# Optimization experiments

Measured on AMD Instinct MI355X. Metric: run time of the kernel, lower is better.

The kernel has to match this reference:

```python
import jax, jax.numpy as jnp
import numpy as np

B, N, H, E, OBS, A, AFF, EFF = 2, 50000, 64, 1_000_000, 128, 18, 512, 256


def setup_inputs() -> dict:
    key = jax.random.key(0)
    ks = jax.random.split(key, 20)
    s = 0.05  # small init to keep gates/tanh unsaturated
    return {
        "obs": jax.random.normal(ks[0], (B, OBS), jnp.float32),
        "state": jax.random.normal(ks[1], (B, N, H), jnp.float32) * 0.1,
        "W_in": jax.random.normal(ks[2], (OBS, H), jnp.float32) * s,
        "b_in": jnp.zeros((H,), jnp.float32),
        "W_msg": jax.random.normal(ks[3], (H, H), jnp.float32) * s,
        "W_gate": jax.random.normal(ks[4], (2 * H, H), jnp.float32) * s,
        "b_gate": jnp.zeros((H,), jnp.float32),
        "W_cand": jax.random.normal(ks[5], (2 * H, H), jnp.float32) * s,
        "b_cand": jnp.zeros((H,), jnp.float32),
        "W_dec": jax.random.normal(ks[6], (H, H), jnp.float32) * s,
        "b_dec": jnp.zeros((H,), jnp.float32),
        "W_mean": jax.random.normal(ks[7], (H, A), jnp.float32) * s,
        "b_mean": jnp.zeros((A,), jnp.float32),
        "W_ls": jax.random.normal(ks[8], (H, A), jnp.float32) * s,
        "b_ls": jnp.zeros((A,), jnp.float32),
        "src_index": jax.random.randint(ks[9], (E,), 0, N),
        "dst_index": jax.random.randint(ks[10], (E,), 0, N),
        "afferent_idx": jax.random.randint(ks[11], (AFF,), 0, N),
        "efferent_idx": jax.random.randint(ks[12], (EFF,), 0, N),
    }


def reference(obs, state, W_in, b_in, W_msg, W_gate, b_gate, W_cand, b_cand,
              W_dec, b_dec, W_mean, b_mean, W_ls, b_ls,
              src_index, dst_index, afferent_idx, efferent_idx):
    # inject obs projection into afferent node slots
    projected = obs @ W_in + b_in                                   # [B, H]
    injected = jnp.zeros_like(state).at[:, afferent_idx, :].set(projected[:, None, :])
    # gather-project-scatter message passing over the edge list
    src_msgs = state[:, src_index, :] @ W_msg                       # [B, E, H]
    messages = jnp.zeros_like(state).at[:, dst_index, :].add(src_msgs)
    # GRU-style gated update
    combined = messages + injected
    gate_in = jnp.concatenate([state, combined], axis=-1)           # [B, N, 2H]
    z = jax.nn.sigmoid(gate_in @ W_gate + b_gate)
    cand = jnp.tanh(gate_in @ W_cand + b_cand)
    next_state = (1.0 - z) * state + z * cand
    # mean-pool readout over efferent nodes, then policy heads
    readout = next_state[:, efferent_idx, :].mean(axis=1)           # [B, H]
    decoded = jnp.tanh(readout @ W_dec + b_dec)
    mean = decoded @ W_mean + b_mean
    log_std = jnp.clip(decoded @ W_ls + b_ls, -5.0, 2.0)
    return mean, log_std, next_state
```

## Files before the change

### kernel.cpp

```cpp
#include <hip/hip_runtime.h>
#include <hip/hip_bf16.h>

constexpr int kN   = 50000;
constexpr int kH   = 64;
constexpr int kB   = 2;
constexpr int kE   = 1000000;
constexpr int kObs = 128;
constexpr int kA   = 18;
constexpr int kAff = 512;
constexpr int kEff = 256;
constexpr int kNH  = kN * kH;
constexpr int kOutOff = 2 * kB * kA;
constexpr int kRanges = 8;
constexpr int kNr  = kN / kRanges;
constexpr int kChunks = 64;
constexpr int kEc  = kE / kChunks;
constexpr int kHistB = kRanges * kChunks;
constexpr int kPackBlocks = (kNH + 8191) / 8192;
constexpr int kWprepBlocks = 20;
constexpr int kScanB = (kN + 255) / 256;

typedef __attribute__((ext_vector_type(8))) short short8_t;
typedef __attribute__((ext_vector_type(4))) float f32x4_t;

__device__ __forceinline__ float ldf(const void* p, int i, int f32) {
  if (f32) return ((const float*)p)[i];
  unsigned short u = ((const unsigned short*)p)[i];
  union { unsigned int x; float f; } v; v.x = ((unsigned int)u) << 16; return v.f;
}
__device__ __forceinline__ void stf(void* p, int i, float val, int f32) {
  if (f32) ((float*)p)[i] = val;
  else ((__hip_bfloat16*)p)[i] = __float2bfloat16(val);
}
__device__ __forceinline__ float lo16(unsigned int w) {
  union { unsigned int i; float f; } v; v.i = w << 16; return v.f;
}
__device__ __forceinline__ float hi16(unsigned int w) {
  union { unsigned int i; float f; } v; v.i = w & 0xffff0000u; return v.f;
}
__device__ __forceinline__ unsigned int f2b(float f) {
  union { float f; unsigned int u; } v; v.f = f;
  unsigned int r = v.u + 0x7fffu + ((v.u >> 16) & 1u);
  return r >> 16;
}
__device__ __forceinline__ int detect64(const unsigned short* wprobe, int t) {
  int hits = 0;
  for (int k = 0; k < 4; ++k) {
    unsigned short u = wprobe[(t * 4 + k) * 2];
    int e = (u >> 7) & 0xFF;
    if ((u & 0x7FFFu) != 0 && e >= 108 && e <= 128) hits++;
  }
  for (int off = 32; off; off >>= 1) hits += __shfl_down(hits, off);
  return (hits < 128) ? 1 : 0;
}

extern "C" __global__ __launch_bounds__(1024) void k_prep(
    const unsigned short* __restrict__ wprobe,
    const void* __restrict__ obs,
    const void* __restrict__ W_in,
    const void* __restrict__ b_in,
    const int* __restrict__ aff_idx,
    const int* __restrict__ dst,
    const void* __restrict__ W_msg,
    const void* __restrict__ W_gate,
    const void* __restrict__ W_cand,
    int* __restrict__ dflag,
    int* __restrict__ flags,
    float* __restrict__ projected,
    int* __restrict__ deg_c,
    unsigned short* __restrict__ wt) {
  __shared__ int sdeg[kNr];
  int t = threadIdx.x, b = blockIdx.x;
  if (b == 0) {
    __shared__ int sflag;
    if (t < 64) { int f = detect64(wprobe, t); if (t == 0) { sflag = f; dflag[0] = f; } }
    for (int i = t; i < kN; i += 1024) flags[i] = 0;
    __syncthreads();
    int f32 = sflag;
    if (t < kAff) flags[aff_idx[t]] = 1;
    if (t < kB * kH) {
      int bb = t >> 6, h = t & 63;
      float acc = ldf(b_in, h, f32);
      for (int o = 0; o < kObs; ++o)
        acc += ldf(obs, bb * kObs + o, f32) * ldf(W_in, o * kH + h, f32);
      projected[t] = acc;
    }
  } else if (b <= kHistB) {
    int h = b - 1, r = h & 7, c = h >> 3;
    int r0 = r * kNr;
    for (int i = t; i < kNr; i += 1024) sdeg[i] = 0;
    __syncthreads();
    int end = (c + 1) * kEc;
    for (int e = c * kEc + t; e < end; e += 1024) {
      unsigned rel = (unsigned)(dst[e] - r0);
      if (rel < (unsigned)kNr) atomicAdd(&sdeg[rel], 1);
    }
    __syncthreads();
    for (int i = t; i < kNr; i += 1024) deg_c[c * kN + r0 + i] = sdeg[i];
  } else {
    __shared__ int sflag;
    if (t < 64) { int f = detect64(wprobe, t); if (t == 0) sflag = f; }
    __syncthreads();
    int f32 = sflag;
    int i = (b - 1 - kHistB) * 1024 + t;
    if (i < 4096) {
      int n = i >> 6, k = i & 63;
      wt[i] = (unsigned short)f2b(ldf(W_msg, k * 64 + n, f32));
    } else if (i < 12288) {
      int j = i - 4096; int n = j >> 7, k = j & 127;
      wt[i] = (unsigned short)f2b(ldf(W_gate, k * 64 + n, f32));
    } else if (i < 20480) {
      int j = i - 12288; int n = j >> 7, k = j & 127;
      wt[i] = (unsigned short)f2b(ldf(W_cand, k * 64 + n, f32));
    }
  }
}

extern "C" __global__ void k_scan1(const int* __restrict__ deg_c,
                                   int* __restrict__ row_off,
                                   int* __restrict__ partials) {
  __shared__ int sd[256];
  int t = threadIdx.x;
  int n = blockIdx.x * 256 + t;
  int s = 0;
  if (n < kN) {
    for (int c = 0; c < kChunks; ++c) s += deg_c[c * kN + n];
  }
  sd[t] = s;
  __syncthreads();
  for (int off = 1; off < 256; off <<= 1) {
    int v = (t >= off) ? sd[t - off] : 0;
    __syncthreads();
    sd[t] += v;
    __syncthreads();
  }
  int excl = sd[t] - s;
  if (t == 255) partials[blockIdx.x] = sd[255];
  if (n < kN) row_off[n] = excl;
}

extern "C" __global__ void k_scan3(int* __restrict__ row_off,
                                   const int* __restrict__ partials,
                                   int* __restrict__ deg_c) {
  __shared__ int sd[256];
  int t = threadIdx.x;
  int s = 0;
  for (int j = t; j < (int)blockIdx.x; j += 256) s += partials[j];
  sd[t] = s;
  __syncthreads();
  for (int off = 128; off; off >>= 1) {
    if (t < off) sd[t] += sd[t + off];
    __syncthreads();
  }
  int base = sd[0];
  int n = blockIdx.x * 256 + t;
  if (n < kN) {
    int v = row_off[n] + base;
    row_off[n] = v;
    int run = v;
#pragma unroll 8
    for (int c = 0; c < kChunks; ++c) {
      int d = deg_c[c * kN + n];
      deg_c[c * kN + n] = run;
      run += d;
    }
  }
  if (blockIdx.x == 0 && t == 0) row_off[kN] = kE;
}

extern "C" __global__ __launch_bounds__(1024) void k_scatter(
    const int* __restrict__ src,
    const int* __restrict__ dst,
    const int* __restrict__ chunk_base,
    int* __restrict__ sorted_src,
    const unsigned short* __restrict__ wprobe,
    const void* __restrict__ state,
    unsigned int* __restrict__ pack) {
  __shared__ int scur[kNr];
  int t = threadIdx.x;
  if (blockIdx.x < kHistB) {
    int r = blockIdx.x & 7, c = blockIdx.x >> 3;
    int r0 = r * kNr;
    for (int i = t; i < kNr; i += 1024) scur[i] = chunk_base[c * kN + r0 + i];
    __syncthreads();
    int end = (c + 1) * kEc;
    for (int e = c * kEc + t; e < end; e += 1024) {
      unsigned rel = (unsigned)(dst[e] - r0);
      if (rel < (unsigned)kNr) {
        int pos = atomicAdd(&scur[rel], 1);
        sorted_src[pos] = src[e];
      }
    }
  } else {
    __shared__ int sflag;
    if (t < 64) { int f = detect64(wprobe, t); if (t == 0) sflag = f; }
    __syncthreads();
    int f32 = sflag;
    int i = (blockIdx.x - kHistB) * 8192 + t * 8;
    if (i < kNH) {
      uint4 o0, o1;
      if (!f32) {
        uint4 a = *(const uint4*)((const unsigned short*)state + i);
        uint4 c4 = *(const uint4*)((const unsigned short*)state + kNH + i);
        o0.x = (a.x & 0xffffu) | (c4.x << 16);
        o0.y = (a.x >> 16)     | (c4.x & 0xffff0000u);
        o0.z = (a.y & 0xffffu) | (c4.y << 16);
        o0.w = (a.y >> 16)     | (c4.y & 0xffff0000u);
        o1.x = (a.z & 0xffffu) | (c4.z << 16);
        o1.y = (a.z >> 16)     | (c4.z & 0xffff0000u);
        o1.z = (a.w & 0xffffu) | (c4.w << 16);
        o1.w = (a.w >> 16)     | (c4.w & 0xffff0000u);
      } else {
        const float* sf = (const float*)state;
        unsigned int w[8];
#pragma unroll
        for (int k = 0; k < 8; ++k)
          w[k] = f2b(sf[i + k]) | (f2b(sf[kNH + i + k]) << 16);
        o0 = make_uint4(w[0], w[1], w[2], w[3]);
        o1 = make_uint4(w[4], w[5], w[6], w[7]);
      }
      *(uint4*)&pack[i] = o0;
      *(uint4*)&pack[i + 4] = o1;
    }
  }
}

extern "C" __global__ __launch_bounds__(256) void k_gather(
    const unsigned int* __restrict__ pack,
    const int* __restrict__ row_off,
    const int* __restrict__ sorted_src,
    unsigned int* __restrict__ agg) {
  int wave = threadIdx.x >> 6, lane = threadIdx.x & 63;
  int n = blockIdx.x * 4 + wave;
  if (n >= kN) return;
  int s  = row_off[n];
  int en = row_off[n + 1];
  int g = lane >> 4, col = lane & 15;
  const uint4* pk4 = (const uint4*)pack;
  float a0x = 0.f, a0y = 0.f, a0z = 0.f, a0w = 0.f;
  float a1x = 0.f, a1y = 0.f, a1z = 0.f, a1w = 0.f;
  for (int e = s; e < en; e += 8) {
#pragma unroll
    for (int h = 0; h < 2; ++h) {
      int ee = e + h * 4 + g;
      int idx = sorted_src[min(ee, en - 1)];
      uint4 wv = pk4[idx * 16 + col];
      if (ee >= en) { wv.x = 0u; wv.y = 0u; wv.z = 0u; wv.w = 0u; }
      a0x += lo16(wv.x); a1x += hi16(wv.x);
      a0y += lo16(wv.y); a1y += hi16(wv.y);
      a0z += lo16(wv.z); a1z += hi16(wv.z);
      a0w += lo16(wv.w); a1w += hi16(wv.w);
    }
  }
  a0x += __shfl_xor(a0x, 16); a0x += __shfl_xor(a0x, 32);
  a0y += __shfl_xor(a0y, 16); a0y += __shfl_xor(a0y, 32);
  a0z += __shfl_xor(a0z, 16); a0z += __shfl_xor(a0z, 32);
  a0w += __shfl_xor(a0w, 16); a0w += __shfl_xor(a0w, 32);
  a1x += __shfl_xor(a1x, 16); a1x += __shfl_xor(a1x, 32);
  a1y += __shfl_xor(a1y, 16); a1y += __shfl_xor(a1y, 32);
  a1z += __shfl_xor(a1z, 16); a1z += __shfl_xor(a1z, 32);
  a1w += __shfl_xor(a1w, 16); a1w += __shfl_xor(a1w, 32);
  if (g == 0) {
    uint4 o;
    o.x = f2b(a0x) | (f2b(a1x) << 16);
    o.y = f2b(a0y) | (f2b(a1y) << 16);
    o.z = f2b(a0z) | (f2b(a1z) << 16);
    o.w = f2b(a0w) | (f2b(a1w) << 16);
    ((uint4*)agg)[n * 16 + col] = o;
  }
}

extern "C" __global__ __launch_bounds__(256) void k_update(
    const unsigned int* __restrict__ pk,
    const unsigned short* __restrict__ wt,
    const void* __restrict__ b_gate,
    const void* __restrict__ b_cand,
    const unsigned int* __restrict__ agg,
    const int* __restrict__ flags,
    const float* __restrict__ projected,
    const int* __restrict__ dflag,
    void* __restrict__ out) {
  __shared__ uint4 lx4[1088];
  __shared__ float sbias[128];
  __shared__ float sproj[128];
  __shared__ int   sfl[32];
  unsigned short* lx  = (unsigned short*)lx4;
  int f32 = dflag[0];
  int t = threadIdx.x;
  int nd0 = blockIdx.x * 32;

  const uint4* pk4 = (const uint4*)pk;
  const uint4* ag4 = (const uint4*)agg;
  for (int i = t; i < 512; i += 256) {
    int ndl = i >> 4, c4 = i & 15;
    int ndg = min(nd0 + ndl, kN - 1);
    uint4 pv = pk4[ndg * 16 + c4];
    uint4 av = ag4[ndg * 16 + c4];
    *(uint2*)&lx[(2 * ndl) * 136 + c4 * 4] =
        make_uint2((pv.x & 0xffffu) | (pv.y << 16), (pv.z & 0xffffu) | (pv.w << 16));
    *(uint2*)&lx[(2 * ndl + 1) * 136 + c4 * 4] =
        make_uint2((pv.x >> 16) | (pv.y & 0xffff0000u), (pv.z >> 16) | (pv.w & 0xffff0000u));
    *(uint2*)&lx[(2 * ndl) * 136 + 64 + c4 * 4] =
        make_uint2((av.x & 0xffffu) | (av.y << 16), (av.z & 0xffffu) | (av.w << 16));
    *(uint2*)&lx[(2 * ndl + 1) * 136 + 64 + c4 * 4] =
        make_uint2((av.x >> 16) | (av.y & 0xffff0000u), (av.z >> 16) | (av.w & 0xffff0000u));
  }
  if (t < 64) sbias[t] = ldf(b_gate, t, f32);
  else if (t < 128) sbias[t] = ldf(b_cand, t - 64, f32);
  else sproj[t - 128] = projected[t - 128];
  if (t < 32) sfl[t] = (nd0 + t < kN) ? flags[nd0 + t] : 0;
  __syncthreads();

  int w = t >> 6, lane = t & 63;
  int q = lane >> 4, l15 = lane & 15;
  int rowb = w * 16;
  const unsigned short* wm = wt;
  const unsigned short* wg = wt + 4096;
  const unsigned short* wc = wt + 12288;

  short8_t a0 = *(const short8_t*)&lx[(rowb + l15) * 136 + 64 + q * 8];
  short8_t a1 = *(const short8_t*)&lx[(rowb + l15) * 136 + 96 + q * 8];
  f32x4_t msgc[4];
#pragma unroll
  for (int ct = 0; ct < 4; ++ct) {
    f32x4_t acc = {0.f, 0.f, 0.f, 0.f};
    short8_t b0 = *(const short8_t*)&wm[(ct * 16 + l15) * 64 + q * 8];
    short8_t b1 = *(const short8_t*)&wm[(ct * 16 + l15) * 64 + 32 + q * 8];
    acc = __builtin_amdgcn_mfma_f32_16x16x32_bf16(a0, b0, acc, 0, 0, 0);
    acc = __builtin_amdgcn_mfma_f32_16x16x32_bf16(a1, b1, acc, 0, 0, 0);
    msgc[ct] = acc;
  }
#pragma unroll
  for (int ct = 0; ct < 4; ++ct) {
    int col = ct * 16 + l15;
    float pj0 = sproj[col], pj1 = sproj[64 + col];
#pragma unroll
    for (int r = 0; r < 4; ++r) {
      int row = rowb + q * 4 + r;
      int ndl = row >> 1, b = row & 1;
      float inj = sfl[ndl] ? (b ? pj1 : pj0) : 0.f;
      lx[row * 136 + 64 + col] = (unsigned short)f2b(msgc[ct][r] + inj);
    }
  }

  short8_t xa[4];
#pragma unroll
  for (int ks = 0; ks < 4; ++ks)
    xa[ks] = *(const short8_t*)&lx[(rowb + l15) * 136 + ks * 32 + q * 8];
#pragma unroll
  for (int ct = 0; ct < 4; ++ct) {
    f32x4_t accg = {0.f, 0.f, 0.f, 0.f}, accc = {0.f, 0.f, 0.f, 0.f};
#pragma unroll
    for (int ks = 0; ks < 4; ++ks) {
      short8_t bg = *(const short8_t*)&wg[(ct * 16 + l15) * 128 + ks * 32 + q * 8];
      short8_t bc = *(const short8_t*)&wc[(ct * 16 + l15) * 128 + ks * 32 + q * 8];
      accg = __builtin_amdgcn_mfma_f32_16x16x32_bf16(xa[ks], bg, accg, 0, 0, 0);
      accc = __builtin_amdgcn_mfma_f32_16x16x32_bf16(xa[ks], bc, accc, 0, 0, 0);
    }
    int col = ct * 16 + l15;
    float bgv = sbias[col], bcv = sbias[64 + col];
#pragma unroll
    for (int rp = 0; rp < 2; ++rp) {
      int rowe = rowb + q * 4 + 2 * rp;
      int nd = nd0 + (rowe >> 1);
      if (nd >= kN) continue;
      unsigned int pv = pk[nd * 64 + col];
      float z0 = 1.f / (1.f + __expf(-(accg[2 * rp] + bgv)));
      float c0 = tanhf(accc[2 * rp] + bcv);
      stf(out, kOutOff + nd * 64 + col, (1.f - z0) * lo16(pv) + z0 * c0, f32);
      float z1 = 1.f / (1.f + __expf(-(accg[2 * rp + 1] + bgv)));
      float c1 = tanhf(accc[2 * rp + 1] + bcv);
      stf(out, kOutOff + kNH + nd * 64 + col, (1.f - z1) * hi16(pv) + z1 * c1, f32);
    }
  }
}

extern "C" __global__ void k_readout(const void* __restrict__ W_dec,
                                     const void* __restrict__ b_dec,
                                     const void* __restrict__ W_mean,
                                     const void* __restrict__ b_mean,
                                     const void* __restrict__ W_ls,
                                     const void* __restrict__ b_ls,
                                     const int* __restrict__ eff_idx,
                                     const int* __restrict__ dflag,
                                     void* __restrict__ out) {
  __shared__ float part[8][64];
  __shared__ float ro[128], dec[128];
  int f32 = dflag[0];
  int t = threadIdx.x;
  int wv = t >> 6, lane = t & 63;
  int b = wv >> 2, g = wv & 3;
  float acc = 0.f;
#pragma unroll 4
  for (int i = 0; i < 64; ++i) {
    int n = eff_idx[g * 64 + i];
    acc += ldf(out, kOutOff + b * kNH + n * 64 + lane, f32);
  }
  part[wv][lane] = acc;
  __syncthreads();
  if (t < 128) {
    int bb = t >> 6, h = t & 63;
    float s = part[bb * 4 + 0][h] + part[bb * 4 + 1][h] +
              part[bb * 4 + 2][h] + part[bb * 4 + 3][h];
    ro[t] = s * (1.f / kEff);
  }
  __syncthreads();
  if (t < 128) {
    int bb = t >> 6, h = t & 63;
    float d = ldf(b_dec, h, f32);
    for (int k = 0; k < 64; ++k) d += ro[bb * 64 + k] * ldf(W_dec, k * 64 + h, f32);
    dec[t] = tanhf(d);
  }
  __syncthreads();
  if (t < kB * kA) {
    int bb = t / kA, a = t % kA;
    float m = ldf(b_mean, a, f32), l = ldf(b_ls, a, f32);
    for (int k = 0; k < 64; ++k) {
      float dv = dec[bb * 64 + k];
      m += dv * ldf(W_mean, k * kA + a, f32);
      l += dv * ldf(W_ls, k * kA + a, f32);
    }
    l = fminf(fmaxf(l, -5.f), 2.f);
    stf(out, t, m, f32);
    stf(out, kB * kA + t, l, f32);
  }
}

extern "C" void kernel_launch(void* const* d_in, const int* in_sizes, int n_in,
                              void* d_out, int out_size, void* d_ws, size_t ws_size,
                              hipStream_t stream) {
  (void)in_sizes; (void)n_in; (void)out_size; (void)ws_size;
  const void* obs    = d_in[0];
  const void* state  = d_in[1];
  const void* W_in   = d_in[2];
  const void* b_in   = d_in[3];
  const void* W_msg  = d_in[4];
  const void* W_gate = d_in[5];
  const void* b_gate = d_in[6];
  const void* W_cand = d_in[7];
  const void* b_cand = d_in[8];
  const void* W_dec  = d_in[9];
  const void* b_dec  = d_in[10];
  const void* W_mean = d_in[11];
  const void* b_mean = d_in[12];
  const void* W_ls   = d_in[13];
  const void* b_ls   = d_in[14];
  const int* src = (const int*)d_in[15];
  const int* dst = (const int*)d_in[16];
  const int* aff = (const int*)d_in[17];
  const int* eff = (const int*)d_in[18];

  int* wsp        = (int*)d_ws;
  int* flags      = wsp;
  int* deg_c      = flags + kN;
  int* row_off    = deg_c + kChunks * kN;
  int* partials   = row_off + (kN + 64);
  int* dflag      = partials + 512;
  float* projected = (float*)(dflag + 16);
  int* sorted_src  = (int*)(projected + 128);
  unsigned int* pk  = (unsigned int*)(sorted_src + kE);
  unsigned int* agg = pk + kNH;
  unsigned short* wt = (unsigned short*)(agg + kNH);

  k_prep<<<1 + kHistB + kWprepBlocks, 1024, 0, stream>>>(
      (const unsigned short*)W_cand, obs, W_in, b_in, aff, dst,
      W_msg, W_gate, W_cand, dflag, flags, projected, deg_c, wt);
  k_scan1<<<kScanB, 256, 0, stream>>>(deg_c, row_off, partials);
  k_scan3<<<kScanB, 256, 0, stream>>>(row_off, partials, deg_c);
  k_scatter<<<kHistB + kPackBlocks, 1024, 0, stream>>>(
      src, dst, deg_c, sorted_src, (const unsigned short*)W_cand, state, pk);
  k_gather<<<(kN + 3) / 4, 256, 0, stream>>>(pk, row_off, sorted_src, agg);
  k_update<<<(kN + 31) / 32, 256, 0, stream>>>(pk, wt, b_gate, b_cand,
                                               agg, flags, projected, dflag, d_out);
  k_readout<<<1, 512, 0, stream>>>(W_dec, b_dec, W_mean, b_mean, W_ls, b_ls, eff,
                                   dflag, d_out);
}
```

Before: 281.1 us.

## Fuse CSR gather into update kernel and stage outputs through LDS

The separate gather kernel is removed. Each wave of the update kernel now aggregates neighbor states for its own 8 nodes directly into LDS, so the intermediate agg buffer no longer has to be written to and read back from global memory. Outputs are staged in LDS and written with coalesced vector stores, and fast rcp-based sigmoid and tanh replace the exact versions. The risks are lower parallelism during the gather phase, since one wave now walks 8 nodes serially, and slightly different rounding from the approximate transcendentals.

```diff
diff --git a/kernel.cpp b/kernel.cpp
--- a/kernel.cpp
+++ b/kernel.cpp
@@ -38,10 +38,19 @@
 __device__ __forceinline__ float hi16(unsigned int w) {
   union { unsigned int i; float f; } v; v.i = w & 0xffff0000u; return v.f;
 }
+__device__ __forceinline__ float b2f(unsigned short u) {
+  union { unsigned int i; float f; } v; v.i = ((unsigned int)u) << 16; return v.f;
+}
 __device__ __forceinline__ unsigned int f2b(float f) {
   union { float f; unsigned int u; } v; v.f = f;
   unsigned int r = v.u + 0x7fffu + ((v.u >> 16) & 1u);
   return r >> 16;
+}
+__device__ __forceinline__ float fsig(float x) {
+  return __builtin_amdgcn_rcpf(1.f + __expf(-x));
+}
+__device__ __forceinline__ float ftanh(float x) {
+  return 1.f - 2.f * __builtin_amdgcn_rcpf(__expf(2.f * x) + 1.f);
 }
 __device__ __forceinline__ int detect64(const unsigned short* wprobe, int t) {
   int hits = 0;
@@ -225,95 +234,75 @@
   }
 }
 
-extern "C" __global__ __launch_bounds__(256) void k_gather(
-    const unsigned int* __restrict__ pack,
-    const int* __restrict__ row_off,
-    const int* __restrict__ sorted_src,
-    unsigned int* __restrict__ agg) {
-  int wave = threadIdx.x >> 6, lane = threadIdx.x & 63;
-  int n = blockIdx.x * 4 + wave;
-  if (n >= kN) return;
-  int s  = row_off[n];
-  int en = row_off[n + 1];
-  int g = lane >> 4, col = lane & 15;
-  const uint4* pk4 = (const uint4*)pack;
-  float a0x = 0.f, a0y = 0.f, a0z = 0.f, a0w = 0.f;
-  float a1x = 0.f, a1y = 0.f, a1z = 0.f, a1w = 0.f;
-  for (int e = s; e < en; e += 8) {
-#pragma unroll
-    for (int h = 0; h < 2; ++h) {
-      int ee = e + h * 4 + g;
-      int idx = sorted_src[min(ee, en - 1)];
-      uint4 wv = pk4[idx * 16 + col];
-      if (ee >= en) { wv.x = 0u; wv.y = 0u; wv.z = 0u; wv.w = 0u; }
-      a0x += lo16(wv.x); a1x += hi16(wv.x);
-      a0y += lo16(wv.y); a1y += hi16(wv.y);
-      a0z += lo16(wv.z); a1z += hi16(wv.z);
-      a0w += lo16(wv.w); a1w += hi16(wv.w);
-    }
-  }
-  a0x += __shfl_xor(a0x, 16); a0x += __shfl_xor(a0x, 32);
-  a0y += __shfl_xor(a0y, 16); a0y += __shfl_xor(a0y, 32);
-  a0z += __shfl_xor(a0z, 16); a0z += __shfl_xor(a0z, 32);
-  a0w += __shfl_xor(a0w, 16); a0w += __shfl_xor(a0w, 32);
-  a1x += __shfl_xor(a1x, 16); a1x += __shfl_xor(a1x, 32);
-  a1y += __shfl_xor(a1y, 16); a1y += __shfl_xor(a1y, 32);
-  a1z += __shfl_xor(a1z, 16); a1z += __shfl_xor(a1z, 32);
-  a1w += __shfl_xor(a1w, 16); a1w += __shfl_xor(a1w, 32);
-  if (g == 0) {
-    uint4 o;
-    o.x = f2b(a0x) | (f2b(a1x) << 16);
-    o.y = f2b(a0y) | (f2b(a1y) << 16);
-    o.z = f2b(a0z) | (f2b(a1z) << 16);
-    o.w = f2b(a0w) | (f2b(a1w) << 16);
-    ((uint4*)agg)[n * 16 + col] = o;
-  }
-}
-
 extern "C" __global__ __launch_bounds__(256) void k_update(
     const unsigned int* __restrict__ pk,
     const unsigned short* __restrict__ wt,
     const void* __restrict__ b_gate,
     const void* __restrict__ b_cand,
-    const unsigned int* __restrict__ agg,
+    const int* __restrict__ row_off,
+    const int* __restrict__ sorted_src,
     const int* __restrict__ flags,
     const float* __restrict__ projected,
     const int* __restrict__ dflag,
     void* __restrict__ out) {
   __shared__ uint4 lx4[1088];
-  __shared__ float sbias[128];
-  __shared__ float sproj[128];
-  __shared__ int   sfl[32];
-  unsigned short* lx  = (unsigned short*)lx4;
+  unsigned short* lx = (unsigned short*)lx4;
   int f32 = dflag[0];
   int t = threadIdx.x;
-  int nd0 = blockIdx.x * 32;
-
-  const uint4* pk4 = (const uint4*)pk;
-  const uint4* ag4 = (const uint4*)agg;
-  for (int i = t; i < 512; i += 256) {
-    int ndl = i >> 4, c4 = i & 15;
-    int ndg = min(nd0 + ndl, kN - 1);
-    uint4 pv = pk4[ndg * 16 + c4];
-    uint4 av = ag4[ndg * 16 + c4];
-    *(uint2*)&lx[(2 * ndl) * 136 + c4 * 4] =
-        make_uint2((pv.x & 0xffffu) | (pv.y << 16), (pv.z & 0xffffu) | (pv.w << 16));
-    *(uint2*)&lx[(2 * ndl + 1) * 136 + c4 * 4] =
-        make_uint2((pv.x >> 16) | (pv.y & 0xffff0000u), (pv.z >> 16) | (pv.w & 0xffff0000u));
-    *(uint2*)&lx[(2 * ndl) * 136 + 64 + c4 * 4] =
-        make_uint2((av.x & 0xffffu) | (av.y << 16), (av.z & 0xffffu) | (av.w << 16));
-    *(uint2*)&lx[(2 * ndl + 1) * 136 + 64 + c4 * 4] =
-        make_uint2((av.x >> 16) | (av.y & 0xffff0000u), (av.z >> 16) | (av.w & 0xffff0000u));
-  }
-  if (t < 64) sbias[t] = ldf(b_gate, t, f32);
-  else if (t < 128) sbias[t] = ldf(b_cand, t - 64, f32);
-  else sproj[t - 128] = projected[t - 128];
-  if (t < 32) sfl[t] = (nd0 + t < kN) ? flags[nd0 + t] : 0;
-  __syncthreads();
-
   int w = t >> 6, lane = t & 63;
   int q = lane >> 4, l15 = lane & 15;
   int rowb = w * 16;
+  int nd0 = blockIdx.x * 32;
+  int ndw = nd0 + w * 8;
+
+  const uint4* pk4 = (const uint4*)pk;
+  for (int j = lane; j < 128; j += 64) {
+    int ndl = j >> 4, c4 = j & 15;
+    int ndg = min(ndw + ndl, kN - 1);
+    uint4 pv = pk4[ndg * 16 + c4];
+    int r0 = rowb + 2 * ndl;
+    *(uint2*)&lx[r0 * 136 + c4 * 4] =
+        make_uint2((pv.x & 0xffffu) | (pv.y << 16), (pv.z & 0xffffu) | (pv.w << 16));
+    *(uint2*)&lx[(r0 + 1) * 136 + c4 * 4] =
+        make_uint2((pv.x >> 16) | (pv.y & 0xffff0000u), (pv.z >> 16) | (pv.w & 0xffff0000u));
+  }
+
+  for (int ndl = 0; ndl < 8; ++ndl) {
+    int n = ndw + ndl;
+    if (n >= kN) break;
+    int s = row_off[n], en = row_off[n + 1];
+    float a0x = 0.f, a0y = 0.f, a0z = 0.f, a0w = 0.f;
+    float a1x = 0.f, a1y = 0.f, a1z = 0.f, a1w = 0.f;
+    for (int e = s; e < en; e += 8) {
+#pragma unroll
+      for (int h = 0; h < 2; ++h) {
+        int ee = e + h * 4 + q;
+        int idx = sorted_src[min(ee, en - 1)];
+        uint4 wv = pk4[idx * 16 + l15];
+        if (ee >= en) { wv.x = 0u; wv.y = 0u; wv.z = 0u; wv.w = 0u; }
+        a0x += lo16(wv.x); a1x += hi16(wv.x);
+        a0y += lo16(wv.y); a1y += hi16(wv.y);
+        a0z += lo16(wv.z); a1z += hi16(wv.z);
+        a0w += lo16(wv.w); a1w += hi16(wv.w);
+      }
+    }
+    a0x += __shfl_xor(a0x, 16); a0x += __shfl_xor(a0x, 32);
+    a0y += __shfl_xor(a0y, 16); a0y += __shfl_xor(a0y, 32);
+    a0z += __shfl_xor(a0z, 16); a0z += __shfl_xor(a0z, 32);
+    a0w += __shfl_xor(a0w, 16); a0w += __shfl_xor(a0w, 32);
+    a1x += __shfl_xor(a1x, 16); a1x += __shfl_xor(a1x, 32);
+    a1y += __shfl_xor(a1y, 16); a1y += __shfl_xor(a1y, 32);
+    a1z += __shfl_xor(a1z, 16); a1z += __shfl_xor(a1z, 32);
+    a1w += __shfl_xor(a1w, 16); a1w += __shfl_xor(a1w, 32);
+    if (q == 0) {
+      int r0 = rowb + 2 * ndl;
+      *(uint2*)&lx[r0 * 136 + 64 + l15 * 4] =
+          make_uint2(f2b(a0x) | (f2b(a0y) << 16), f2b(a0z) | (f2b(a0w) << 16));
+      *(uint2*)&lx[(r0 + 1) * 136 + 64 + l15 * 4] =
+          make_uint2(f2b(a1x) | (f2b(a1y) << 16), f2b(a1z) | (f2b(a1w) << 16));
+    }
+  }
+
   const unsigned short* wm = wt;
   const unsigned short* wg = wt + 4096;
   const unsigned short* wc = wt + 12288;
@@ -330,15 +319,18 @@
     acc = __builtin_amdgcn_mfma_f32_16x16x32_bf16(a1, b1, acc, 0, 0, 0);
     msgc[ct] = acc;
   }
+  int nA = nd0 + w * 8 + q * 2, nB = nA + 1;
+  int flA = (nA < kN) ? flags[nA] : 0;
+  int flB = (nB < kN) ? flags[nB] : 0;
 #pragma unroll
   for (int ct = 0; ct < 4; ++ct) {
     int col = ct * 16 + l15;
-    float pj0 = sproj[col], pj1 = sproj[64 + col];
+    float pj0 = projected[col], pj1 = projected[64 + col];
 #pragma unroll
     for (int r = 0; r < 4; ++r) {
       int row = rowb + q * 4 + r;
-      int ndl = row >> 1, b = row & 1;
-      float inj = sfl[ndl] ? (b ? pj1 : pj0) : 0.f;
+      int fl = (r < 2) ? flA : flB;
+      float inj = fl ? ((row & 1) ? pj1 : pj0) : 0.f;
       lx[row * 136 + 64 + col] = (unsigned short)f2b(msgc[ct][r] + inj);
     }
   }
@@ -347,6 +339,16 @@
 #pragma unroll
   for (int ks = 0; ks < 4; ++ks)
     xa[ks] = *(const short8_t*)&lx[(rowb + l15) * 136 + ks * 32 + q * 8];
+  float ps[16];
+#pragma unroll
+  for (int ct = 0; ct < 4; ++ct)
+#pragma unroll
+    for (int rp = 0; rp < 2; ++rp) {
+      int row = rowb + q * 4 + 2 * rp;
+      ps[ct * 4 + rp * 2 + 0] = b2f(lx[row * 136 + ct * 16 + l15]);
+      ps[ct * 4 + rp * 2 + 1] = b2f(lx[(row + 1) * 136 + ct * 16 + l15]);
+    }
+  float* soutw = (float*)((char*)lx4 + w * 4352);
 #pragma unroll
   for (int ct = 0; ct < 4; ++ct) {
     f32x4_t accg = {0.f, 0.f, 0.f, 0.f}, accc = {0.f, 0.f, 0.f, 0.f};
@@ -358,20 +360,48 @@
       accc = __builtin_amdgcn_mfma_f32_16x16x32_bf16(xa[ks], bc, accc, 0, 0, 0);
     }
     int col = ct * 16 + l15;
-    float bgv = sbias[col], bcv = sbias[64 + col];
+    float bgv = ldf(b_gate, col, f32), bcv = ldf(b_cand, col, f32);
 #pragma unroll
     for (int rp = 0; rp < 2; ++rp) {
-      int rowe = rowb + q * 4 + 2 * rp;
-      int nd = nd0 + (rowe >> 1);
-      if (nd >= kN) continue;
-      unsigned int pv = pk[nd * 64 + col];
-      float z0 = 1.f / (1.f + __expf(-(accg[2 * rp] + bgv)));
-      float c0 = tanhf(accc[2 * rp] + bcv);
-      stf(out, kOutOff + nd * 64 + col, (1.f - z0) * lo16(pv) + z0 * c0, f32);
-      float z1 = 1.f / (1.f + __expf(-(accg[2 * rp + 1] + bgv)));
-      float c1 = tanhf(accc[2 * rp + 1] + bcv);
-      stf(out, kOutOff + kNH + nd * 64 + col, (1.f - z1) * hi16(pv) + z1 * c1, f32);
-    }
+      int r = q * 4 + 2 * rp;
+      float z0 = fsig(accg[2 * rp] + bgv);
+      float c0 = ftanh(accc[2 * rp] + bcv);
+      soutw[r * 64 + col] = (1.f - z0) * ps[ct * 4 + rp * 2 + 0] + z0 * c0;
+      float z1 = fsig(accg[2 * rp + 1] + bgv);
+      float c1 = ftanh(accc[2 * rp + 1] + bcv);
+      soutw[(r + 1) * 64 + col] = (1.f - z1) * ps[ct * 4 + rp * 2 + 1] + z1 * c1;
+    }
+  }
+  __syncthreads();
+
+  int nvalid = min(32, kN - nd0) * 64;
+  if (f32) {
+    float* po = (float*)out + kOutOff;
+#pragma unroll
+    for (int p = 0; p < 2; ++p)
+      for (int j = t * 4; j < nvalid; j += 1024) {
+        int ndl = j >> 6, c = j & 63;
+        int wv = ndl >> 3, r = ((ndl & 7) << 1) + p;
+        float4 v = *(float4*)((char*)lx4 + wv * 4352 + r * 256 + c * 4);
+        *(float4*)(po + p * kNH + nd0 * 64 + j) = v;
+      }
+  } else {
+    unsigned short* po = (unsigned short*)out + kOutOff;
+#pragma unroll
+    for (int p = 0; p < 2; ++p)
+      for (int j = t * 8; j < nvalid; j += 2048) {
+        int ndl = j >> 6, c = j & 63;
+        int wv = ndl >> 3, r = ((ndl & 7) << 1) + p;
+        const char* base = (const char*)lx4 + wv * 4352 + r * 256 + c * 4;
+        float4 v0 = *(const float4*)base;
+        float4 v1 = *(const float4*)(base + 16);
+        uint4 o;
+        o.x = f2b(v0.x) | (f2b(v0.y) << 16);
+        o.y = f2b(v0.z) | (f2b(v0.w) << 16);
+        o.z = f2b(v1.x) | (f2b(v1.y) << 16);
+        o.w = f2b(v1.z) | (f2b(v1.w) << 16);
+        *(uint4*)(po + p * kNH + nd0 * 64 + j) = o;
+      }
   }
 }
 
@@ -459,8 +489,7 @@
   float* projected = (float*)(dflag + 16);
   int* sorted_src  = (int*)(projected + 128);
   unsigned int* pk  = (unsigned int*)(sorted_src + kE);
-  unsigned int* agg = pk + kNH;
-  unsigned short* wt = (unsigned short*)(agg + kNH);
+  unsigned short* wt = (unsigned short*)(pk + kNH);
 
   k_prep<<<1 + kHistB + kWprepBlocks, 1024, 0, stream>>>(
       (const unsigned short*)W_cand, obs, W_in, b_in, aff, dst,
@@ -469,9 +498,9 @@
   k_scan3<<<kScanB, 256, 0, stream>>>(row_off, partials, deg_c);
   k_scatter<<<kHistB + kPackBlocks, 1024, 0, stream>>>(
       src, dst, deg_c, sorted_src, (const unsigned short*)W_cand, state, pk);
-  k_gather<<<(kN + 3) / 4, 256, 0, stream>>>(pk, row_off, sorted_src, agg);
   k_update<<<(kN + 31) / 32, 256, 0, stream>>>(pk, wt, b_gate, b_cand,
-                                               agg, flags, projected, dflag, d_out);
+                                               row_off, sorted_src, flags,
+                                               projected, dflag, d_out);
   k_readout<<<1, 512, 0, stream>>>(W_dec, b_dec, W_mean, b_mean, W_ls, b_ls, eff,
                                    dflag, d_out);
 }
```

Result: no change. 281.1 us (+0.0%).
